# Performance work log

Measured on AMD Instinct MI355X. Metric: run time of the kernel, lower is better.

## Reference

```python
import jax, jax.numpy as jnp
import numpy as np

B, T, DIM, H, DH, DT = 2, 2048, 1024, 16, 64, 32
Q_TEMP, K_TEMP = 1.0, 1.0
EPS = float(np.finfo(np.float32).eps)  # torch RMSNorm default eps for fp32
INV_SQRT_DH = 1.0 / np.sqrt(DH)


def _get_time(length, head_time_delta, time_angles, with_time_delta):
    # [T,1,1] positions, optionally offset per head -> [T,H,1]
    pos = jnp.arange(length, dtype=jnp.float32)[:, None, None]
    if with_time_delta:
        pos = pos + head_time_delta[None, :, None]          # [T,H,1]
    else:
        pos = jnp.broadcast_to(pos, (length, H, 1))          # [T,H,1]
    ang = pos * time_angles                                  # [T,H,Dt]
    c, s = jnp.cos(ang), jnp.sin(ang)
    return jnp.concatenate([c + s, c - s], axis=-1) * INV_SQRT_DH  # [T,H,2Dt]


def setup_inputs() -> dict:
    key = jax.random.key(0)
    ks = jax.random.split(key, 6)
    sc = 0.02
    states = jax.random.normal(ks[0], (B, T, DIM), jnp.float32)
    attention_mask = jnp.ones((B, T), jnp.int32)
    ln_w = jnp.ones((DIM,), jnp.float32)
    time_angles = 10000.0 ** (-1.0 / jnp.arange(1, DT + 1, dtype=jnp.float32))
    head_time_delta = jax.random.uniform(ks[1], (H,), jnp.float32)
    Wq = jax.random.normal(ks[2], (H * DH, DIM), jnp.float32) * sc
    q_bias = jnp.zeros((H * DH,), jnp.float32)
    Wk = jax.random.normal(ks[3], (H * DH, DIM), jnp.float32) * sc
    bk = jnp.zeros((H * DH,), jnp.float32)
    Wv = jax.random.normal(ks[4], (H * DH, DIM), jnp.float32) * sc
    bv = jnp.zeros((H * DH,), jnp.float32)
    Wo = jax.random.normal(ks[5], (DIM, H * DH), jnp.float32) * sc
    bo = jnp.zeros((DIM,), jnp.float32)
    return dict(states=states, attention_mask=attention_mask, ln_w=ln_w,
                time_angles=time_angles, head_time_delta=head_time_delta,
                Wq=Wq, q_bias=q_bias, Wk=Wk, bk=bk, Wv=Wv, bv=bv, Wo=Wo, bo=bo)


def reference(states, attention_mask, ln_w, time_angles, head_time_delta,
              Wq, q_bias, Wk, bk, Wv, bv, Wo, bo):
    # RMSNorm
    x = states * jax.lax.rsqrt(jnp.mean(states * states, axis=-1, keepdims=True) + EPS) * ln_w
    m = attention_mask.astype(x.dtype)[:, :, None, None]   # [B,T,1,1]

    # Q path -> q_attentioned [B,T,T,H]
    q = (x @ Wq.T - jnp.exp(q_bias)).reshape(B, T, H, DH)
    q_sm = jax.nn.softmax(q / Q_TEMP * m, axis=-1)
    t_q = _get_time(T, head_time_delta, time_angles, True)   # [T,H,2Dt]
    t_k = _get_time(T, head_time_delta, time_angles, False)  # [T,H,2Dt]
    q_timed = jnp.sum(q_sm, axis=-1, keepdims=True) * t_q    # [B,T,H,2Dt]
    q_att = jnp.einsum('bthd,lhd->btlh', q_timed, t_k)       # [B,T,T,H]

    # KV path
    k = (x @ Wk.T + bk).reshape(B, T, H, DH)
    k_sm = jax.nn.softmax(k / K_TEMP * m, axis=-1)
    v = (x @ Wv.T + bv).reshape(B, T, H, DH)
    kv = k_sm * v                                            # [B,T,H,Dh]

    loading = jnp.einsum('btlh,blhd->bthd', q_att, kv)       # [B,T,H,Dh]
    return loading.reshape(B, T, DIM) @ Wo.T + bo
```

## Files before the change

kernel.cpp:

```cpp
#include <hip/hip_runtime.h>
#include <math.h>

#define T_ 2048
#define H_ 16

typedef __attribute__((ext_vector_type(8))) short bfx8;
typedef __attribute__((ext_vector_type(4))) float f32x4;

__device__ __forceinline__ short f2bf(float f) {
  union { float f; unsigned u; } x; x.f = f;
  unsigned r = (x.u + 0x7FFFu + ((x.u >> 16) & 1u)) >> 16;
  return (short)r;
}
__device__ __forceinline__ float bf2f(short s) {
  union { unsigned u; float f; } x;
  x.u = ((unsigned)(unsigned short)s) << 16;
  return x.f;
}

#define GLD_LDS(g, l) \
  __builtin_amdgcn_global_load_lds( \
      (const __attribute__((address_space(1))) void*)(g), \
      (__attribute__((address_space(3))) void*)(l), 16, 0, 0)

__global__ __launch_bounds__(256) void prep_kernel(
    const float* __restrict__ Wk, const float* __restrict__ Wv,
    const float* __restrict__ Wo, const float* __restrict__ angles,
    const float* __restrict__ states, const float* __restrict__ ln_w,
    short* __restrict__ Wkb, short* __restrict__ Wvb, short* __restrict__ Wob,
    short* __restrict__ xb, short* __restrict__ Cb, short* __restrict__ tkT) {
  const int blk = blockIdx.x;
  if (blk < 3072) {
    const int i = blk * 256 + threadIdx.x;
    const int which = i >> 18;
    const int idx = i & 262143;
    const float* s = (which == 0) ? Wk : (which == 1) ? Wv : Wo;
    short* d = (which == 0) ? Wkb : (which == 1) ? Wvb : Wob;
    const float4 v = ((const float4*)s)[idx];
    short4 r;
    r.x = f2bf(v.x); r.y = f2bf(v.y); r.z = f2bf(v.z); r.w = f2bf(v.w);
    ((short4*)d)[idx] = r;
  } else if (blk < 7168) {
    const int row = blk - 3072;
    const int tid = threadIdx.x;
    const float4 v = ((const float4*)(states + (size_t)row * 1024))[tid];
    float ss = v.x * v.x + v.y * v.y + v.z * v.z + v.w * v.w;
#pragma unroll
    for (int off = 32; off >= 1; off >>= 1) ss += __shfl_xor(ss, off);
    __shared__ float red[4];
    if ((tid & 63) == 0) red[tid >> 6] = ss;
    __syncthreads();
    const float tot = red[0] + red[1] + red[2] + red[3];
    const float scale = rsqrtf(tot * (1.0f / 1024.0f) + 1.1920928955078125e-07f);
    const float4 w = ((const float4*)ln_w)[tid];
    short4 o;
    o.x = f2bf(v.x * scale * w.x);
    o.y = f2bf(v.y * scale * w.y);
    o.z = f2bf(v.z * scale * w.z);
    o.w = f2bf(v.w * scale * w.w);
    ((short4*)(xb + (size_t)row * 1024))[tid] = o;
  } else if (blk < 7424) {
    const int gid = (blk - 7168) * 256 + threadIdx.x;
    const int j = gid & 31;
    const int t = gid >> 5;
    float s, c;
    sincosf((float)t * angles[j], &s, &c);
    Cb[(size_t)t * 64 + j] = f2bf(0.125f * c);
    Cb[(size_t)t * 64 + 32 + j] = f2bf(0.125f * s);
  } else {
    const int gid = (blk - 7424) * 256 + threadIdx.x;
    const int tc = gid & 255;
    const int j = gid >> 8;
    const float th = angles[j];
    short lo[8], hi[8];
#pragma unroll
    for (int r = 0; r < 8; ++r) {
      float s, c;
      sincosf((float)(tc * 8 + r) * th, &s, &c);
      lo[r] = f2bf((c + s) * 0.125f);
      hi[r] = f2bf((c - s) * 0.125f);
    }
    short* base = tkT + (size_t)j * 2048 + tc * 8;
    *(short4*)(base) = *(short4*)&lo[0];
    *(short4*)(base + 4) = *(short4*)&lo[4];
    short* base2 = tkT + (size_t)(32 + j) * 2048 + tc * 8;
    *(short4*)(base2) = *(short4*)&hi[0];
    *(short4*)(base2 + 4) = *(short4*)&hi[4];
  }
}

__global__ __launch_bounds__(256) void kvgemm_kernel(
    const short* __restrict__ xb, const short* __restrict__ Wkb,
    const short* __restrict__ Wvb, const float* __restrict__ bk,
    const float* __restrict__ bv, const int* __restrict__ mask,
    const short* __restrict__ tkT, float* __restrict__ Mt) {
  __shared__ short smem[8192];
  __shared__ short Vs[128][64];
  short(*As)[32] = (short(*)[32])smem;
  short(*Bk)[32] = (short(*)[32])(smem + 4096);
  short(*Bv)[32] = (short(*)[32])(smem + 6144);
  short(*kvS)[128] = (short(*)[128])smem;

  const int row0 = blockIdx.x * 128;
  const int h = blockIdx.y;
  const int t = threadIdx.x;
  const int lane = t & 63;
  const int wv = t >> 6;
  const bool isV = wv >= 2;
  const int wrow = (wv & 1) * 64;
  const int lrow = lane & 15;
  const int kg = (lane >> 4) * 8;
  const int srow = t >> 2;
  const int skb = (t & 3) * 8;
  const short* ga = xb + (size_t)(row0 + srow) * 1024 + skb;
  const short* gk = Wkb + (size_t)(h * 64 + srow) * 1024 + skb;
  const short* gv = Wvb + (size_t)(h * 64 + srow) * 1024 + skb;

  f32x4 acc[4][4] = {};
  for (int k0 = 0; k0 < 1024; k0 += 32) {
    GLD_LDS(ga + k0, &As[srow][skb]);
    GLD_LDS(ga + 64 * 1024 + k0, &As[64 + srow][skb]);
    GLD_LDS(gk + k0, &Bk[srow][skb]);
    GLD_LDS(gv + k0, &Bv[srow][skb]);
    __syncthreads();
    bfx8 af[4], bf_[4];
#pragma unroll
    for (int i = 0; i < 4; ++i) af[i] = *(const bfx8*)&As[wrow + i * 16 + lrow][kg];
    const short(*Bs)[32] = isV ? Bv : Bk;
#pragma unroll
    for (int j = 0; j < 4; ++j) bf_[j] = *(const bfx8*)&Bs[j * 16 + lrow][kg];
#pragma unroll
    for (int i = 0; i < 4; ++i)
#pragma unroll
      for (int j = 0; j < 4; ++j)
        acc[i][j] = __builtin_amdgcn_mfma_f32_16x16x32_bf16(af[i], bf_[j], acc[i][j], 0, 0, 0);
    __syncthreads();
  }
  const int rq = (lane >> 4) * 4;
  if (isV) {
#pragma unroll
    for (int j = 0; j < 4; ++j) {
      const float bb = bv[h * 64 + j * 16 + lrow];
#pragma unroll
      for (int i = 0; i < 4; ++i)
#pragma unroll
        for (int rr = 0; rr < 4; ++rr)
          Vs[wrow + rq + i * 16 + rr][j * 16 + lrow] = f2bf(acc[i][j][rr] + bb);
    }
  }
  __syncthreads();
  if (!isV) {
    float bkc[4];
#pragma unroll
    for (int j = 0; j < 4; ++j) bkc[j] = bk[h * 64 + j * 16 + lrow];
    const int rowg0 = row0 + wrow + rq;
#pragma unroll
    for (int i = 0; i < 4; ++i) {
#pragma unroll
      for (int rr = 0; rr < 4; ++rr) {
        const float m = (float)mask[rowg0 + i * 16 + rr];
        float kf[4];
#pragma unroll
        for (int j = 0; j < 4; ++j) kf[j] = (acc[i][j][rr] + bkc[j]) * m;
        float mx = fmaxf(fmaxf(kf[0], kf[1]), fmaxf(kf[2], kf[3]));
#pragma unroll
        for (int off = 8; off >= 1; off >>= 1) mx = fmaxf(mx, __shfl_xor(mx, off));
        float s = 0.0f;
#pragma unroll
        for (int j = 0; j < 4; ++j) { kf[j] = expf(kf[j] - mx); s += kf[j]; }
#pragma unroll
        for (int off = 8; off >= 1; off >>= 1) s += __shfl_xor(s, off);
        const float inv = 1.0f / s;
#pragma unroll
        for (int j = 0; j < 4; ++j)
          acc[i][j][rr] = kf[j] * inv *
                          bf2f(Vs[wrow + rq + i * 16 + rr][j * 16 + lrow]);
      }
    }
#pragma unroll
    for (int j = 0; j < 4; ++j) {
      const int d = j * 16 + lrow;
#pragma unroll
      for (int i = 0; i < 4; ++i) {
        short4 o;
        o.x = f2bf(acc[i][j][0]); o.y = f2bf(acc[i][j][1]);
        o.z = f2bf(acc[i][j][2]); o.w = f2bf(acc[i][j][3]);
        *(short4*)&kvS[d][wrow + rq + i * 16] = o;
      }
    }
  }
  __syncthreads();
  const int bb = row0 >> 11;
  const int tb = row0 & 2047;
  const short* tkb = tkT + (size_t)(wv * 16 + lrow) * 2048 + tb;
  f32x4 macc[4] = {};
#pragma unroll
  for (int kc = 0; kc < 4; ++kc) {
    const bfx8 af = *(const bfx8*)(tkb + kc * 32 + kg);
#pragma unroll
    for (int j = 0; j < 4; ++j) {
      const bfx8 bf_ = *(const bfx8*)&kvS[j * 16 + lrow][kc * 32 + kg];
      macc[j] = __builtin_amdgcn_mfma_f32_16x16x32_bf16(af, bf_, macc[j], 0, 0, 0);
    }
  }
  float* Mb = Mt + (size_t)(bb * 16 + h) * 4096;
#pragma unroll
  for (int j = 0; j < 4; ++j) {
    const int d = j * 16 + lrow;
#pragma unroll
    for (int rr = 0; rr < 4; ++rr) {
      const int e = wv * 16 + rq + rr;
      atomicAdd(&Mb[(size_t)e * 64 + d], macc[j][rr]);
    }
  }
}

__global__ __launch_bounds__(256) void fold_kernel(
    const float* __restrict__ Mt, const float* __restrict__ angles,
    const float* __restrict__ delta, short* __restrict__ Mf) {
  const int bh = blockIdx.x;
  const int b = bh >> 4, h = bh & 15;
  const int t = threadIdx.x;
  const int j = t >> 3;
  const int d8 = (t & 7) * 8;
  float sphi, cphi;
  sincosf(delta[h] * angles[j], &sphi, &cphi);
  const float p = cphi + sphi, q = cphi - sphi;
  const float* m0 = Mt + (size_t)bh * 4096 + (size_t)j * 64 + d8;
  const float* m1 = Mt + (size_t)bh * 4096 + (size_t)(32 + j) * 64 + d8;
  short* oc = Mf + (size_t)b * 65536 + (size_t)j * 1024 + h * 64 + d8;
  short* os = Mf + (size_t)b * 65536 + (size_t)(32 + j) * 1024 + h * 64 + d8;
#pragma unroll
  for (int c = 0; c < 8; ++c) {
    const float a = m0[c], bb = m1[c];
    oc[c] = f2bf(p * a + q * bb);
    os[c] = f2bf(q * a - p * bb);
  }
}

__global__ __launch_bounds__(256) void hgemm_kernel(
    const short* __restrict__ Wob, const short* __restrict__ Mf,
    float* __restrict__ H) {
  const int kc = blockIdx.x;
  const int o0 = blockIdx.y * 64;
  const int b = blockIdx.z;
  const int t = threadIdx.x;
  const int lane = t & 63;
  const int w = t >> 6;
  const int lrow = lane & 15;
  const int kg = (lane >> 4) * 8;
  const int orow = o0 + w * 16 + lrow;
  f32x4 acc[4] = {};
#pragma unroll
  for (int it = 0; it < 4; ++it) {
    const int kb = kc * 128 + it * 32 + kg;
    const bfx8 af = *(const bfx8*)(Wob + (size_t)orow * 1024 + kb);
#pragma unroll
    for (int j = 0; j < 4; ++j) {
      const bfx8 bf_ = *(const bfx8*)(Mf + (size_t)b * 65536 +
                                      (size_t)(j * 16 + lrow) * 1024 + kb);
      acc[j] = __builtin_amdgcn_mfma_f32_16x16x32_bf16(af, bf_, acc[j], 0, 0, 0);
    }
  }
  float* Hb = H + (size_t)b * 65536;
#pragma unroll
  for (int j = 0; j < 4; ++j) {
    const int kap = j * 16 + lrow;
#pragma unroll
    for (int rr = 0; rr < 4; ++rr) {
      const int o = o0 + w * 16 + (lane >> 4) * 4 + rr;
      atomicAdd(&Hb[(size_t)o * 64 + kap], acc[j][rr]);
    }
  }
}

__global__ __launch_bounds__(256) void ofinal_kernel(
    const short* __restrict__ Cb, const float* __restrict__ H,
    const float* __restrict__ bo, float* __restrict__ out) {
  const int col0 = blockIdx.x * 128;
  const int row0 = blockIdx.y * 128;
  const int b = blockIdx.z;
  float* C = out + (size_t)b * 2097152;
  const float* Hb = H + (size_t)b * 65536;
  const int t = threadIdx.x;
  const int lane = t & 63;
  const int wv = t >> 6;
  const int wm = (wv & 1) * 64, wn = (wv >> 1) * 64;
  const int lrow = lane & 15;
  const int kg = (lane >> 4) * 8;
  f32x4 acc[4][4] = {};
#pragma unroll
  for (int k0 = 0; k0 < 64; k0 += 32) {
    bfx8 af[4], bf_[4];
#pragma unroll
    for (int i = 0; i < 4; ++i)
      af[i] = *(const bfx8*)(Cb + (size_t)(row0 + wm + i * 16 + lrow) * 64 + k0 + kg);
#pragma unroll
    for (int j = 0; j < 4; ++j) {
      const float* hp = Hb + (size_t)(col0 + wn + j * 16 + lrow) * 64 + k0 + kg;
      const float4 h0 = *(const float4*)hp;
      const float4 h1 = *(const float4*)(hp + 4);
      bfx8 bb;
      bb[0] = f2bf(h0.x); bb[1] = f2bf(h0.y); bb[2] = f2bf(h0.z); bb[3] = f2bf(h0.w);
      bb[4] = f2bf(h1.x); bb[5] = f2bf(h1.y); bb[6] = f2bf(h1.z); bb[7] = f2bf(h1.w);
      bf_[j] = bb;
    }
#pragma unroll
    for (int i = 0; i < 4; ++i)
#pragma unroll
      for (int j = 0; j < 4; ++j)
        acc[i][j] = __builtin_amdgcn_mfma_f32_16x16x32_bf16(af[i], bf_[j], acc[i][j], 0, 0, 0);
  }
  const int rq = (lane >> 4) * 4;
#pragma unroll
  for (int j = 0; j < 4; ++j) {
    const int c = col0 + wn + j * 16 + lrow;
    const float bb = bo[c];
#pragma unroll
    for (int i = 0; i < 4; ++i) {
      const int r = row0 + wm + i * 16 + rq;
#pragma unroll
      for (int rr = 0; rr < 4; ++rr)
        C[(size_t)(r + rr) * 1024 + c] = acc[i][j][rr] + bb;
    }
  }
}

extern "C" void kernel_launch(void* const* d_in, const int* in_sizes, int n_in,
                              void* d_out, int out_size, void* d_ws, size_t ws_size,
                              hipStream_t stream) {
  (void)in_sizes; (void)n_in; (void)out_size; (void)ws_size;
  const float* states = (const float*)d_in[0];
  const int* mask = (const int*)d_in[1];
  const float* ln_w = (const float*)d_in[2];
  const float* angles = (const float*)d_in[3];
  const float* delta = (const float*)d_in[4];
  const float* Wk = (const float*)d_in[7];
  const float* bk = (const float*)d_in[8];
  const float* Wv = (const float*)d_in[9];
  const float* bv = (const float*)d_in[10];
  const float* Wo = (const float*)d_in[11];
  const float* bo = (const float*)d_in[12];
  float* out = (float*)d_out;

  char* W = (char*)d_ws;
  short* xb  = (short*)(W);
  short* Wkb = (short*)(W + (8u << 20));
  short* Wvb = (short*)(W + (10u << 20));
  short* Wob = (short*)(W + (12u << 20));
  short* Cb  = (short*)(W + (14u << 20));
  short* tkT = (short*)(W + (14u << 20) + (256u << 10));
  short* Mf  = (short*)(W + (14u << 20) + (512u << 10));
  float* Mt  = (float*)(W + (15u << 20));
  float* H   = (float*)(W + (15u << 20) + (512u << 10));

  hipMemsetAsync(Mt, 0, (1u << 20), stream);
  prep_kernel<<<7456, 256, 0, stream>>>(Wk, Wv, Wo, angles, states, ln_w,
                                        Wkb, Wvb, Wob, xb, Cb, tkT);
  kvgemm_kernel<<<dim3(32, 16), 256, 0, stream>>>(xb, Wkb, Wvb, bk, bv, mask,
                                                  tkT, Mt);
  fold_kernel<<<32, 256, 0, stream>>>(Mt, angles, delta, Mf);
  hgemm_kernel<<<dim3(8, 16, 2), 256, 0, stream>>>(Wob, Mf, H);
  ofinal_kernel<<<dim3(8, 16, 2), 256, 0, stream>>>(Cb, H, bo, out);
}
```

Baseline: 153.3 us.

## Double K-tile depth with XOR-swizzled LDS in kv GEMM, fold memset into prep

```diff
diff --git a/kernel.cpp b/kernel.cpp
--- a/kernel.cpp
+++ b/kernel.cpp
@@ -28,7 +28,8 @@
     const float* __restrict__ Wo, const float* __restrict__ angles,
     const float* __restrict__ states, const float* __restrict__ ln_w,
     short* __restrict__ Wkb, short* __restrict__ Wvb, short* __restrict__ Wob,
-    short* __restrict__ xb, short* __restrict__ Cb, short* __restrict__ tkT) {
+    short* __restrict__ xb, short* __restrict__ Cb, short* __restrict__ tkT,
+    float* __restrict__ MtH) {
   const int blk = blockIdx.x;
   if (blk < 3072) {
     const int i = blk * 256 + threadIdx.x;
@@ -67,7 +68,7 @@
     sincosf((float)t * angles[j], &s, &c);
     Cb[(size_t)t * 64 + j] = f2bf(0.125f * c);
     Cb[(size_t)t * 64 + 32 + j] = f2bf(0.125f * s);
-  } else {
+  } else if (blk < 7456) {
     const int gid = (blk - 7424) * 256 + threadIdx.x;
     const int tc = gid & 255;
     const int j = gid >> 8;
@@ -86,6 +87,9 @@
     short* base2 = tkT + (size_t)(32 + j) * 2048 + tc * 8;
     *(short4*)(base2) = *(short4*)&hi[0];
     *(short4*)(base2 + 4) = *(short4*)&hi[4];
+  } else {
+    const int gid = (blk - 7456) * 256 + threadIdx.x;
+    ((float4*)MtH)[gid] = make_float4(0.f, 0.f, 0.f, 0.f);
   }
 }
 
@@ -94,12 +98,12 @@
     const short* __restrict__ Wvb, const float* __restrict__ bk,
     const float* __restrict__ bv, const int* __restrict__ mask,
     const short* __restrict__ tkT, float* __restrict__ Mt) {
-  __shared__ short smem[8192];
+  __shared__ short smem[16384];
   __shared__ short Vs[128][64];
-  short(*As)[32] = (short(*)[32])smem;
-  short(*Bk)[32] = (short(*)[32])(smem + 4096);
-  short(*Bv)[32] = (short(*)[32])(smem + 6144);
-  short(*kvS)[128] = (short(*)[128])smem;
+  short(*As)[64] = (short(*)[64])smem;
+  short(*Bk)[64] = (short(*)[64])(smem + 8192);
+  short(*Bv)[64] = (short(*)[64])(smem + 12288);
+  short(*kvS)[132] = (short(*)[132])smem;
 
   const int row0 = blockIdx.x * 128;
   const int h = blockIdx.y;
@@ -109,31 +113,44 @@
   const bool isV = wv >= 2;
   const int wrow = (wv & 1) * 64;
   const int lrow = lane & 15;
-  const int kg = (lane >> 4) * 8;
-  const int srow = t >> 2;
-  const int skb = (t & 3) * 8;
-  const short* ga = xb + (size_t)(row0 + srow) * 1024 + skb;
-  const short* gk = Wkb + (size_t)(h * 64 + srow) * 1024 + skb;
-  const short* gv = Wvb + (size_t)(h * 64 + srow) * 1024 + skb;
+
+  const int srow8 = t >> 3;
+  const int kslotS = (t & 7) ^ (srow8 & 7);
+  const short* gaS = xb + (size_t)(row0 + srow8) * 1024 + kslotS * 8;
+  const short* gkS = Wkb + (size_t)(h * 64 + srow8) * 1024 + kslotS * 8;
+  const short* gvS = Wvb + (size_t)(h * 64 + srow8) * 1024 + kslotS * 8;
+  short* laS = &As[srow8][(t & 7) * 8];
+  short* lkS = &Bk[srow8][(t & 7) * 8];
+  short* lvS = &Bv[srow8][(t & 7) * 8];
 
   f32x4 acc[4][4] = {};
-  for (int k0 = 0; k0 < 1024; k0 += 32) {
-    GLD_LDS(ga + k0, &As[srow][skb]);
-    GLD_LDS(ga + 64 * 1024 + k0, &As[64 + srow][skb]);
-    GLD_LDS(gk + k0, &Bk[srow][skb]);
-    GLD_LDS(gv + k0, &Bv[srow][skb]);
+  for (int k0 = 0; k0 < 1024; k0 += 64) {
+    GLD_LDS(gaS + k0, laS);
+    GLD_LDS(gaS + 32 * 1024 + k0, laS + 2048);
+    GLD_LDS(gaS + 64 * 1024 + k0, laS + 4096);
+    GLD_LDS(gaS + 96 * 1024 + k0, laS + 6144);
+    GLD_LDS(gkS + k0, lkS);
+    GLD_LDS(gkS + 32 * 1024 + k0, lkS + 2048);
+    GLD_LDS(gvS + k0, lvS);
+    GLD_LDS(gvS + 32 * 1024 + k0, lvS + 2048);
     __syncthreads();
-    bfx8 af[4], bf_[4];
-#pragma unroll
-    for (int i = 0; i < 4; ++i) af[i] = *(const bfx8*)&As[wrow + i * 16 + lrow][kg];
-    const short(*Bs)[32] = isV ? Bv : Bk;
-#pragma unroll
-    for (int j = 0; j < 4; ++j) bf_[j] = *(const bfx8*)&Bs[j * 16 + lrow][kg];
-#pragma unroll
-    for (int i = 0; i < 4; ++i)
+#pragma unroll
+    for (int kk = 0; kk < 2; ++kk) {
+      const int pcol = ((kk * 4 + (lane >> 4)) ^ (lrow & 7)) * 8;
+      bfx8 af[4], bf_[4];
+#pragma unroll
+      for (int i = 0; i < 4; ++i)
+        af[i] = *(const bfx8*)&As[wrow + i * 16 + lrow][pcol];
+      const short(*Bs)[64] = isV ? Bv : Bk;
 #pragma unroll
       for (int j = 0; j < 4; ++j)
-        acc[i][j] = __builtin_amdgcn_mfma_f32_16x16x32_bf16(af[i], bf_[j], acc[i][j], 0, 0, 0);
+        bf_[j] = *(const bfx8*)&Bs[j * 16 + lrow][pcol];
+#pragma unroll
+      for (int i = 0; i < 4; ++i)
+#pragma unroll
+        for (int j = 0; j < 4; ++j)
+          acc[i][j] = __builtin_amdgcn_mfma_f32_16x16x32_bf16(af[i], bf_[j], acc[i][j], 0, 0, 0);
+    }
     __syncthreads();
   }
   const int rq = (lane >> 4) * 4;
@@ -193,6 +210,7 @@
   const int bb = row0 >> 11;
   const int tb = row0 & 2047;
   const short* tkb = tkT + (size_t)(wv * 16 + lrow) * 2048 + tb;
+  const int kg = (lane >> 4) * 8;
   f32x4 macc[4] = {};
 #pragma unroll
   for (int kc = 0; kc < 4; ++kc) {
@@ -354,9 +372,8 @@
   float* Mt  = (float*)(W + (15u << 20));
   float* H   = (float*)(W + (15u << 20) + (512u << 10));
 
-  hipMemsetAsync(Mt, 0, (1u << 20), stream);
-  prep_kernel<<<7456, 256, 0, stream>>>(Wk, Wv, Wo, angles, states, ln_w,
-                                        Wkb, Wvb, Wob, xb, Cb, tkT);
+  prep_kernel<<<7712, 256, 0, stream>>>(Wk, Wv, Wo, angles, states, ln_w,
+                                        Wkb, Wvb, Wob, xb, Cb, tkT, Mt);
   kvgemm_kernel<<<dim3(32, 16), 256, 0, stream>>>(xb, Wkb, Wvb, bk, bv, mask,
                                                   tkT, Mt);
   fold_kernel<<<32, 256, 0, stream>>>(Mt, angles, delta, Mf);
```

Measured after the change: 145.0 us. -5.4%, faster.
